# Performance work log

Measured on AMD Instinct MI355X. Metric: run time of the kernel, lower is better.

## Reference

```python
import jax, jax.numpy as jnp
import numpy as np

LAYERS = [3, 1024, 512, 256, 128, 1]
WIDTHS = [3, 1024, 1024, 1024, 1024, 1]  # width per BsPINN: 2^(i-1)*Layers[i]
N = 131072


def _mask(num_blocks, bs1, bs2):
    # block-diagonal mask of ones, built statically (constant under jit)
    return jnp.asarray(np.kron(np.eye(num_blocks, dtype=np.float32),
                               np.ones((bs1, bs2), dtype=np.float32)))


def _xavier(key, shape, fan_in, fan_out):
    lim = np.sqrt(6.0 / (fan_in + fan_out)).astype(np.float32)
    return jax.random.uniform(key, shape, jnp.float32, -lim, lim)


def setup_inputs() -> dict:
    key = jax.random.key(0)
    ks = jax.random.split(key, 6)
    inp = {
        "X": jax.random.uniform(ks[0], (N, 3), dtype=jnp.float32),
        "lb_X": jnp.zeros((3,), jnp.float32),
        "ub_X": jnp.ones((3,), jnp.float32),
    }
    for i in range(5):
        # xavier scale per sub-block Layers[i] x Layers[i+1], as in the torch init
        inp[f"W{i}"] = _xavier(ks[i + 1], (WIDTHS[i], WIDTHS[i + 1]),
                               LAYERS[i], LAYERS[i + 1])
        inp[f"b{i}"] = jnp.zeros((1, WIDTHS[i + 1]), jnp.float32)
    return inp


def reference(X, lb_X, ub_X, W0, b0, W1, b1, W2, b2, W3, b3, W4, b4):
    # masks for hidden layers l=2,3: 2 blocks of 512x512, 4 blocks of 256x256
    m2 = _mask(2, LAYERS[2], 2 * LAYERS[3])   # [1024,1024]
    m3 = _mask(4, LAYERS[3], 2 * LAYERS[4])   # [1024,1024]
    h = 2.0 * (X - lb_X) / (ub_X - lb_X) - 1.0  # [N,3]
    h = jnp.sin(h @ W0 + b0)            # [N,1024] dense
    h = jnp.sin(h @ W1 + b1)            # [N,1024] dense
    h = jnp.sin(h @ (W2 * m2) + b2)     # [N,1024] block-diag (2 blocks)
    h = jnp.sin(h @ (W3 * m3) + b3)     # [N,1024] block-diag (4 blocks)
    return h @ W4 + b4                  # [N,1]
```

## Files before the change

kernel.cpp:

```cpp
#include <hip/hip_runtime.h>

typedef _Float16 f16x8 __attribute__((ext_vector_type(8)));
typedef _Float16 f16x4 __attribute__((ext_vector_type(4)));
typedef __fp16  fp16x2 __attribute__((ext_vector_type(2)));
typedef float f32x4 __attribute__((ext_vector_type(4)));
typedef unsigned int u32;

#define ROWS 64
#define THREADS 512

__global__ __launch_bounds__(512) void pack_weights(
    const float* __restrict__ W1, const float* __restrict__ W2,
    const float* __restrict__ W3, _Float16* __restrict__ WF1,
    _Float16* __restrict__ WF2, _Float16* __restrict__ WF3) {
  int t = blockIdx.x * 512 + threadIdx.x;
  const float* src; _Float16* dst; int idx, ct, kt, lane, kbase;
  if (t < 131072) {
    idx = t; src = W1; dst = WF1;
    ct = idx >> 11; kt = (idx >> 6) & 31; lane = idx & 63; kbase = 0;
  } else if (t < 196608) {
    idx = t - 131072; src = W2; dst = WF2;
    ct = idx >> 10; kt = (idx >> 6) & 15; lane = idx & 63;
    kbase = (ct >= 32) ? 512 : 0;
  } else {
    idx = t - 196608; src = W3; dst = WF3;
    ct = idx >> 9; kt = (idx >> 6) & 7; lane = idx & 63;
    kbase = (ct >> 4) << 8;
  }
  int c  = ct * 16 + (lane & 15);
  int k0 = kbase + kt * 32 + ((lane >> 4) << 3);
  f16x8 v;
#pragma unroll
  for (int j = 0; j < 8; ++j) v[j] = (_Float16)src[(size_t)(k0 + j) * 1024 + c];
  *reinterpret_cast<f16x8*>(dst + (size_t)idx * 8) = v;
}

template <int KT>
__device__ __forceinline__ void layer_mfma(char* hb, const _Float16* __restrict__ WF,
                                           const float* __restrict__ bias,
                                           int wid, int lane, int kbase) {
  f32x4 acc[8][4];
#pragma unroll
  for (int cf = 0; cf < 8; ++cf)
#pragma unroll
    for (int rf = 0; rf < 4; ++rf) acc[cf][rf] = f32x4{0.f, 0.f, 0.f, 0.f};

  const f16x8* wf = reinterpret_cast<const f16x8*>(WF) +
                    (u32)(wid * 8 * KT * 64 + lane);
  const int arow = lane & 15;
  const int koff = (lane >> 4) << 3;
  const u32 abase = (u32)(arow * 2048);
  const u32 axor  = (u32)((arow & 7) << 4);

  f16x8 wA[8], wB[8], hA[4], hB[4];
#define LOADW(buf, ktv)                                                        \
  { u32 _kt = (u32)(ktv);                                                      \
    _Pragma("unroll") for (int cf = 0; cf < 8; ++cf)                           \
      buf[cf] = wf[(u32)(cf * KT) * 64u + _kt * 64u]; }
#define LDH(buf, ktv)                                                          \
  { u32 kb = (u32)((kbase + (ktv) * 32 + koff) * 2);                           \
    _Pragma("unroll") for (int rf = 0; rf < 4; ++rf) {                         \
      u32 addr = ((u32)(rf * 32768) + abase + kb) ^ axor;                      \
      buf[rf] = *reinterpret_cast<const f16x8*>(hb + addr);                    \
    } }
#define DOMFMA(w, h)                                                           \
  { __builtin_amdgcn_s_setprio(1);                                             \
    _Pragma("unroll") for (int cf = 0; cf < 8; ++cf)                           \
      _Pragma("unroll") for (int rf = 0; rf < 4; ++rf)                         \
        acc[cf][rf] = __builtin_amdgcn_mfma_f32_16x16x32_f16(w[cf], h[rf],     \
                                                             acc[cf][rf], 0, 0, 0); \
    __builtin_amdgcn_s_setprio(0); }

  LOADW(wA, 0);
  LDH(hA, 0);
#pragma unroll 1
  for (int kt = 0; kt < KT; kt += 2) {
    int ktn = (kt + 2 < KT) ? (kt + 2) : 0;
    LOADW(wB, kt + 1);
    LDH(hB, kt + 1);
    DOMFMA(wA, hA);
    LOADW(wA, ktn);
    LDH(hA, ktn);
    DOMFMA(wB, hB);
  }
#undef LOADW
#undef LDH
#undef DOMFMA

  __syncthreads();
  const int csub = (lane >> 4) << 2;
  const int rr   = lane & 15;
#pragma unroll
  for (int cf = 0; cf < 8; ++cf) {
    int c0 = wid * 128 + cf * 16 + csub;
    f32x4 bb = *reinterpret_cast<const f32x4*>(bias + c0);
#pragma unroll
    for (int rf = 0; rf < 4; ++rf) {
      int r = rf * 16 + rr;
      float s0 = __sinf(acc[cf][rf][0] + bb[0]);
      float s1 = __sinf(acc[cf][rf][1] + bb[1]);
      float s2 = __sinf(acc[cf][rf][2] + bb[2]);
      float s3 = __sinf(acc[cf][rf][3] + bb[3]);
      union { fp16x2 h2[2]; f16x4 v; } pk;
      pk.h2[0] = __builtin_amdgcn_cvt_pkrtz(s0, s1);
      pk.h2[1] = __builtin_amdgcn_cvt_pkrtz(s2, s3);
      u32 addr = ((u32)(r * 2048 + c0 * 2)) ^ ((u32)((r & 7) << 4));
      *reinterpret_cast<f16x4*>(hb + addr) = pk.v;
    }
  }
  __syncthreads();
}

__global__
__attribute__((amdgpu_flat_work_group_size(512, 512), amdgpu_waves_per_eu(2, 2)))
void bspinn_fused(
    const float* __restrict__ X, const float* __restrict__ lb,
    const float* __restrict__ ub,
    const float* __restrict__ W0, const float* __restrict__ b0,
    const _Float16* __restrict__ WF1, const float* __restrict__ b1,
    const _Float16* __restrict__ WF2, const float* __restrict__ b2,
    const _Float16* __restrict__ WF3, const float* __restrict__ b3,
    const float* __restrict__ W4, const float* __restrict__ b4,
    float* __restrict__ out) {
  __shared__ alignas(16) char hb[ROWS * 2048];
  __shared__ float xs[ROWS * 4];
  __shared__ float partials[ROWS * 8];

  const int tid  = threadIdx.x;
  const int lane = tid & 63;
  const int wid  = tid >> 6;
  const int r0   = blockIdx.x * ROWS;

  if (tid < ROWS * 3) {
    int r = tid / 3, j = tid - r * 3;
    float x = X[(size_t)r0 * 3 + tid];
    xs[r * 4 + j] = 2.0f * (x - lb[j]) / (ub[j] - lb[j]) - 1.0f;
  }
  __syncthreads();

  {
    int c0 = tid * 2;
    float wa0 = W0[c0],        wb0 = W0[c0 + 1];
    float wa1 = W0[1024 + c0], wb1 = W0[1025 + c0];
    float wa2 = W0[2048 + c0], wb2 = W0[2049 + c0];
    float ba = b0[c0], bbv = b0[c0 + 1];
#pragma unroll 4
    for (int r = 0; r < ROWS; ++r) {
      float x0 = xs[r * 4], x1 = xs[r * 4 + 1], x2 = xs[r * 4 + 2];
      float va = __sinf(fmaf(x2, wa2, fmaf(x1, wa1, fmaf(x0, wa0, ba))));
      float vb = __sinf(fmaf(x2, wb2, fmaf(x1, wb1, fmaf(x0, wb0, bbv))));
      union { fp16x2 h2; u32 u; } pk;
      pk.h2 = __builtin_amdgcn_cvt_pkrtz(va, vb);
      u32 addr = ((u32)(r * 2048 + c0 * 2)) ^ ((u32)((r & 7) << 4));
      *reinterpret_cast<u32*>(hb + addr) = pk.u;
    }
  }
  __syncthreads();

  layer_mfma<32>(hb, WF1, b1, wid, lane, 0);
  layer_mfma<16>(hb, WF2, b2, wid, lane, (wid >> 2) * 512);
  layer_mfma<8 >(hb, WF3, b3, wid, lane, (wid >> 1) * 256);

  {
    int r = lane, seg = wid;
    u32 rb = (u32)(r * 2048);
    u32 xr = (u32)((r & 7) << 4);
    float s = 0.f;
#pragma unroll
    for (int kk = 0; kk < 128; kk += 8) {
      int k = seg * 128 + kk;
      f16x8 v = *reinterpret_cast<const f16x8*>(hb + ((rb + (u32)(k * 2)) ^ xr));
#pragma unroll
      for (int j = 0; j < 8; ++j) s = fmaf((float)v[j], W4[k + j], s);
    }
    partials[seg * 64 + r] = s;
  }
  __syncthreads();
  if (tid < ROWS) {
    float s = b4[0];
#pragma unroll
    for (int g = 0; g < 8; ++g) s += partials[g * 64 + tid];
    out[r0 + tid] = s;
  }
}

extern "C" void kernel_launch(void* const* d_in, const int* in_sizes, int n_in,
                              void* d_out, int out_size, void* d_ws, size_t ws_size,
                              hipStream_t stream) {
  const float* X  = (const float*)d_in[0];
  const float* lb = (const float*)d_in[1];
  const float* ub = (const float*)d_in[2];
  const float* W0 = (const float*)d_in[3];
  const float* b0 = (const float*)d_in[4];
  const float* W1 = (const float*)d_in[5];
  const float* b1 = (const float*)d_in[6];
  const float* W2 = (const float*)d_in[7];
  const float* b2 = (const float*)d_in[8];
  const float* W3 = (const float*)d_in[9];
  const float* b3 = (const float*)d_in[10];
  const float* W4 = (const float*)d_in[11];
  const float* b4 = (const float*)d_in[12];
  float* out = (float*)d_out;

  _Float16* WF1 = (_Float16*)d_ws;
  _Float16* WF2 = (_Float16*)((char*)d_ws + 2097152);
  _Float16* WF3 = (_Float16*)((char*)d_ws + 2097152 + 1048576);

  hipLaunchKernelGGL(pack_weights, dim3(448), dim3(512), 0, stream,
                     W1, W2, W3, WF1, WF2, WF3);
  hipLaunchKernelGGL(bspinn_fused, dim3(131072 / ROWS), dim3(THREADS), 0, stream,
                     X, lb, ub, W0, b0, WF1, b1, WF2, b2, WF3, b3, W4, b4, out);
}
```

Measured before the change: 491.4 us.

## Split each wave's column tile into two halves to cut accumulator registers

```diff
diff --git a/kernel.cpp b/kernel.cpp
--- a/kernel.cpp
+++ b/kernel.cpp
@@ -35,37 +35,31 @@
   *reinterpret_cast<f16x8*>(dst + (size_t)idx * 8) = v;
 }
 
-template <int KT>
-__device__ __forceinline__ void layer_mfma(char* hb, const _Float16* __restrict__ WF,
-                                           const float* __restrict__ bias,
-                                           int wid, int lane, int kbase) {
-  f32x4 acc[8][4];
-#pragma unroll
-  for (int cf = 0; cf < 8; ++cf)
-#pragma unroll
-    for (int rf = 0; rf < 4; ++rf) acc[cf][rf] = f32x4{0.f, 0.f, 0.f, 0.f};
-
+template <int KTFULL>
+__device__ __forceinline__ void kloop(const _Float16* __restrict__ WF, char* hb,
+                                      f32x4 (&acc)[4][4], int ct0, int lane,
+                                      int nkt, u32 ldsk0) {
   const f16x8* wf = reinterpret_cast<const f16x8*>(WF) +
-                    (u32)(wid * 8 * KT * 64 + lane);
+                    (u32)(ct0 * KTFULL * 64 + lane);
   const int arow = lane & 15;
   const int koff = (lane >> 4) << 3;
   const u32 abase = (u32)(arow * 2048);
   const u32 axor  = (u32)((arow & 7) << 4);
 
-  f16x8 wA[8], wB[8], hA[4], hB[4];
+  f16x8 wA[4], wB[4], hA[4], hB[4];
 #define LOADW(buf, ktv)                                                        \
   { u32 _kt = (u32)(ktv);                                                      \
-    _Pragma("unroll") for (int cf = 0; cf < 8; ++cf)                           \
-      buf[cf] = wf[(u32)(cf * KT) * 64u + _kt * 64u]; }
+    _Pragma("unroll") for (int cf = 0; cf < 4; ++cf)                           \
+      buf[cf] = wf[(u32)(cf * KTFULL) * 64u + _kt * 64u]; }
 #define LDH(buf, ktv)                                                          \
-  { u32 kb = (u32)((kbase + (ktv) * 32 + koff) * 2);                           \
+  { u32 kb = ldsk0 + (u32)((ktv) * 64) + (u32)(koff * 2);                      \
     _Pragma("unroll") for (int rf = 0; rf < 4; ++rf) {                         \
       u32 addr = ((u32)(rf * 32768) + abase + kb) ^ axor;                      \
       buf[rf] = *reinterpret_cast<const f16x8*>(hb + addr);                    \
     } }
 #define DOMFMA(w, h)                                                           \
   { __builtin_amdgcn_s_setprio(1);                                             \
-    _Pragma("unroll") for (int cf = 0; cf < 8; ++cf)                           \
+    _Pragma("unroll") for (int cf = 0; cf < 4; ++cf)                           \
       _Pragma("unroll") for (int rf = 0; rf < 4; ++rf)                         \
         acc[cf][rf] = __builtin_amdgcn_mfma_f32_16x16x32_f16(w[cf], h[rf],     \
                                                              acc[cf][rf], 0, 0, 0); \
@@ -74,8 +68,8 @@
   LOADW(wA, 0);
   LDH(hA, 0);
 #pragma unroll 1
-  for (int kt = 0; kt < KT; kt += 2) {
-    int ktn = (kt + 2 < KT) ? (kt + 2) : 0;
+  for (int kt = 0; kt < nkt; kt += 2) {
+    int ktn = (kt + 2 < nkt) ? (kt + 2) : 0;
     LOADW(wB, kt + 1);
     LDH(hB, kt + 1);
     DOMFMA(wA, hA);
@@ -86,29 +80,6 @@
 #undef LOADW
 #undef LDH
 #undef DOMFMA
-
-  __syncthreads();
-  const int csub = (lane >> 4) << 2;
-  const int rr   = lane & 15;
-#pragma unroll
-  for (int cf = 0; cf < 8; ++cf) {
-    int c0 = wid * 128 + cf * 16 + csub;
-    f32x4 bb = *reinterpret_cast<const f32x4*>(bias + c0);
-#pragma unroll
-    for (int rf = 0; rf < 4; ++rf) {
-      int r = rf * 16 + rr;
-      float s0 = __sinf(acc[cf][rf][0] + bb[0]);
-      float s1 = __sinf(acc[cf][rf][1] + bb[1]);
-      float s2 = __sinf(acc[cf][rf][2] + bb[2]);
-      float s3 = __sinf(acc[cf][rf][3] + bb[3]);
-      union { fp16x2 h2[2]; f16x4 v; } pk;
-      pk.h2[0] = __builtin_amdgcn_cvt_pkrtz(s0, s1);
-      pk.h2[1] = __builtin_amdgcn_cvt_pkrtz(s2, s3);
-      u32 addr = ((u32)(r * 2048 + c0 * 2)) ^ ((u32)((r & 7) << 4));
-      *reinterpret_cast<f16x4*>(hb + addr) = pk.v;
-    }
-  }
-  __syncthreads();
 }
 
 __global__
@@ -124,7 +95,7 @@
     float* __restrict__ out) {
   __shared__ alignas(16) char hb[ROWS * 2048];
   __shared__ float xs[ROWS * 4];
-  __shared__ float partials[ROWS * 8];
+  __shared__ float partials[8 * ROWS];
 
   const int tid  = threadIdx.x;
   const int lane = tid & 63;
@@ -157,9 +128,79 @@
   }
   __syncthreads();
 
-  layer_mfma<32>(hb, WF1, b1, wid, lane, 0);
-  layer_mfma<16>(hb, WF2, b2, wid, lane, (wid >> 2) * 512);
-  layer_mfma<8 >(hb, WF3, b3, wid, lane, (wid >> 1) * 256);
+  const int csub = (lane >> 4) << 2;
+  const int rr   = lane & 15;
+  f32x4 acc[4][4];
+  f16x4 p1[4][4], p2[4][4];
+
+  auto zacc = [&]() {
+#pragma unroll
+    for (int cf = 0; cf < 4; ++cf)
+#pragma unroll
+      for (int rf = 0; rf < 4; ++rf) acc[cf][rf] = f32x4{0.f, 0.f, 0.f, 0.f};
+  };
+  auto epi_regs = [&](f16x4 (&p)[4][4], const float* bias, int c0w) {
+#pragma unroll
+    for (int cf = 0; cf < 4; ++cf) {
+      int c0 = c0w + cf * 16 + csub;
+      f32x4 bb = *reinterpret_cast<const f32x4*>(bias + c0);
+#pragma unroll
+      for (int rf = 0; rf < 4; ++rf) {
+        float s0 = __sinf(acc[cf][rf][0] + bb[0]);
+        float s1 = __sinf(acc[cf][rf][1] + bb[1]);
+        float s2 = __sinf(acc[cf][rf][2] + bb[2]);
+        float s3 = __sinf(acc[cf][rf][3] + bb[3]);
+        union { fp16x2 h2[2]; f16x4 v; } pk;
+        pk.h2[0] = __builtin_amdgcn_cvt_pkrtz(s0, s1);
+        pk.h2[1] = __builtin_amdgcn_cvt_pkrtz(s2, s3);
+        p[cf][rf] = pk.v;
+      }
+    }
+  };
+  auto store_regs = [&](f16x4 (&p)[4][4], int c0w) {
+#pragma unroll
+    for (int cf = 0; cf < 4; ++cf) {
+      int c0 = c0w + cf * 16 + csub;
+#pragma unroll
+      for (int rf = 0; rf < 4; ++rf) {
+        int r = rf * 16 + rr;
+        u32 addr = ((u32)(r * 2048 + c0 * 2)) ^ ((u32)((r & 7) << 4));
+        *reinterpret_cast<f16x4*>(hb + addr) = p[cf][rf];
+      }
+    }
+  };
+
+  const int cw0 = wid * 64;
+  const int cw1 = 512 + wid * 64;
+  const int ct00 = wid * 4, ct01 = 32 + wid * 4;
+
+  zacc(); kloop<32>(WF1, hb, acc, ct00, lane, 32, 0);
+  epi_regs(p1, b1, cw0);
+  zacc(); kloop<32>(WF1, hb, acc, ct01, lane, 32, 0);
+  epi_regs(p2, b1, cw1);
+  __syncthreads();
+  store_regs(p1, cw0); store_regs(p2, cw1);
+  __syncthreads();
+
+  zacc(); kloop<16>(WF2, hb, acc, ct00, lane, 16, 0);
+  epi_regs(p1, b2, cw0);
+  zacc(); kloop<16>(WF2, hb, acc, ct01, lane, 16, 1024);
+  epi_regs(p2, b2, cw1);
+  __syncthreads();
+  store_regs(p1, cw0); store_regs(p2, cw1);
+  __syncthreads();
+
+  {
+    u32 k0a = (u32)(((wid >> 2)) * 512);
+    u32 k0b = (u32)((2 + (wid >> 2)) * 512);
+    zacc(); kloop<8>(WF3, hb, acc, ct00, lane, 8, k0a);
+    epi_regs(p1, b3, cw0);
+    zacc(); kloop<8>(WF3, hb, acc, ct01, lane, 8, k0b);
+    epi_regs(p2, b3, cw1);
+    __syncthreads();
+    store_regs(p1, cw0); store_regs(p2, cw1);
+    __syncthreads();
+  }
 
   {
     int r = lane, seg = wid;
@@ -204,7 +245,7 @@
 
   _Float16* WF1 = (_Float16*)d_ws;
   _Float16* WF2 = (_Float16*)((char*)d_ws + 2097152);
-  _Float16* WF3 = (_Float16*)((char*)d_ws + 2097152 + 1048576);
+  _Float16* WF3 = (_Float16*)((char*)d_ws + 3145728);
 
   hipLaunchKernelGGL(pack_weights, dim3(448), dim3(512), 0, stream,
                      W1, W2, W3, WF1, WF2, WF3);
```

After: 490.2 us. About the same (-0.2%).
